# Kernel tuning notes

Hardware: AMD Instinct MI355X
Metric: run time of the kernel (lower is better)

## Reference

```python
import jax, jax.numpy as jnp
import numpy as np


def setup_inputs() -> dict:
    key = jax.random.key(0)
    ks = jax.random.split(key, 6)
    B, C, H, W, O = 8, 64, 64, 64, 64
    x = jax.random.normal(ks[0], (B, C, H, W), jnp.float32)
    wq = jax.random.normal(ks[1], (O, C), jnp.float32) * 0.1
    wk = jax.random.normal(ks[2], (O, C), jnp.float32) * 0.1
    wv = jax.random.normal(ks[3], (O, C), jnp.float32) * 0.1
    rel_w = jax.random.normal(ks[4], (O, W), jnp.float32)
    rel_h = jax.random.normal(ks[5], (O, H), jnp.float32)
    return {"x": x, "wq": wq, "wk": wk, "wv": wv,
            "rel_w": rel_w, "rel_h": rel_h,
            "kernel_size": 7, "padding": 3}


def reference(x, wq, wk, wv, rel_w, rel_h, kernel_size, padding):
    B, C, H, W = x.shape
    k, p = kernel_size, padding
    # 1x1 convs (no bias) == channel matmuls
    q = jnp.einsum('bchw,oc->bohw', x, wq)                      # [B,O,H,W]
    xp = jnp.pad(x, ((0, 0), (0, 0), (p, p), (p, p)))
    k_out = jnp.einsum('bchw,oc->bohw', xp, wk)                 # [B,O,H+2p,W+2p]
    v_out = jnp.einsum('bchw,oc->bohw', xp, wv)

    def patches(t):  # torch unfold(2).unfold(3) order: row offset slowest
        return jnp.stack([t[:, :, i:i + H, j:j + W]
                          for i in range(k) for j in range(k)], axis=-1)  # [B,O,H,W,k*k]

    kp = patches(k_out)
    vp = patches(v_out)
    # relative position logits (broadcast elementwise einsums)
    rel = q * rel_w[None, :, None, :] + q * rel_h[None, :, :, None]  # [B,O,H,W]
    logits = q[..., None] * kp + rel[..., None]                 # [B,O,H,W,k*k]
    attn = jax.nn.softmax(logits, axis=-1)
    return jnp.sum(attn * vp, axis=-1)                          # [B,O,H,W]
```

## Files before the change

### kernel.cpp

```cpp
#include <hip/hip_runtime.h>

#define HW 4096

__device__ float g_qkv[3 * 8 * 64 * HW];

#if __has_builtin(__builtin_amdgcn_exp2f)
#define QSCALE 1.4426950408889634f
__device__ __forceinline__ float fexp(float l) { return __builtin_amdgcn_exp2f(l); }
#else
#define QSCALE 1.0f
__device__ __forceinline__ float fexp(float l) { return __expf(l); }
#endif

__global__ __launch_bounds__(256, 2) void qkv_proj(
    const float* __restrict__ x,
    const float* __restrict__ wq,
    const float* __restrict__ wk,
    const float* __restrict__ wv)
{
    __shared__ float xs[64][64];
    __shared__ float wl[3][64][65];
    const int t = threadIdx.x;
    const int b = blockIdx.x >> 6;
    const int h = blockIdx.x & 63;

    {
        const float* __restrict__ mats[3] = { wq, wk, wv };
        #pragma unroll
        for (int m = 0; m < 3; ++m)
            for (int i = t; i < 4096; i += 256) {
                int o = i >> 6, c = i & 63;
                wl[m][o][c] = mats[m][i];
            }
        const float* xrow = x + (size_t)b * 64 * HW + (size_t)h * 64;
        for (int i = t; i < 4096; i += 256) {
            int c = i >> 6, w = i & 63;
            xs[c][w] = xrow[(size_t)c * HW + w];
        }
    }
    __syncthreads();

    const int w0 = (t & 15) * 4;
    const int o0 = (t >> 4) * 4;
    float acc[3][16];
    #pragma unroll
    for (int m = 0; m < 3; ++m)
        #pragma unroll
        for (int i = 0; i < 16; ++i) acc[m][i] = 0.f;

    #pragma unroll 4
    for (int cq = 0; cq < 16; ++cq) {
        const int c0 = cq * 4;
        float xa[4][4];
        #pragma unroll
        for (int ci = 0; ci < 4; ++ci)
            *(float4*)&xa[ci][0] = *(const float4*)&xs[c0 + ci][w0];
        #pragma unroll
        for (int m = 0; m < 3; ++m)
            #pragma unroll
            for (int oi = 0; oi < 4; ++oi) {
                #pragma unroll
                for (int ci = 0; ci < 4; ++ci) {
                    const float wv1 = wl[m][o0 + oi][c0 + ci];
                    #pragma unroll
                    for (int wi = 0; wi < 4; ++wi)
                        acc[m][oi * 4 + wi] = fmaf(wv1, xa[ci][wi], acc[m][oi * 4 + wi]);
                }
            }
    }

    #pragma unroll
    for (int m = 0; m < 3; ++m) {
        float* op = g_qkv + ((size_t)m * 8 + b) * (64 * HW) + (size_t)h * 64 + w0;
        #pragma unroll
        for (int oi = 0; oi < 4; ++oi) {
            float4 v = { acc[m][oi * 4 + 0], acc[m][oi * 4 + 1],
                         acc[m][oi * 4 + 2], acc[m][oi * 4 + 3] };
            *(float4*)&op[(size_t)(o0 + oi) * HW] = v;
        }
    }
}

__global__ __launch_bounds__(256, 2) void attn(float* __restrict__ out)
{
    __shared__ float kv[70][140];
    const int t = threadIdx.x;
    const int b = blockIdx.x >> 6;
    const int o = blockIdx.x & 63;

    const float* qb = g_qkv + ((size_t)(0 * 8 + b) * 64 + o) * HW;
    const float* kb = g_qkv + ((size_t)(1 * 8 + b) * 64 + o) * HW;
    const float* vb = g_qkv + ((size_t)(2 * 8 + b) * 64 + o) * HW;

    for (int i = t; i < 70 * 70; i += 256) {
        int r = i / 70, c = i - r * 70;
        int gh = r - 3, gw = c - 3;
        float kk = 0.f, vv = 0.f;
        if ((unsigned)gh < 64u && (unsigned)gw < 64u) {
            kk = kb[gh * 64 + gw];
            vv = vb[gh * 64 + gw];
        }
        kv[r][c] = kk;
        kv[r][70 + c] = vv;
    }
    __syncthreads();

    const int r0 = (t >> 4) * 4;
    const int c0 = (t & 15) * 4;

    float qv[16], den[16], num[16];
    #pragma unroll
    for (int i = 0; i < 4; ++i) {
        float4 q4 = *(const float4*)&qb[(r0 + i) * 64 + c0];
        qv[i * 4 + 0] = q4.x * QSCALE; qv[i * 4 + 1] = q4.y * QSCALE;
        qv[i * 4 + 2] = q4.z * QSCALE; qv[i * 4 + 3] = q4.w * QSCALE;
    }
    #pragma unroll
    for (int i = 0; i < 16; ++i) { den[i] = 0.f; num[i] = 0.f; }

    #pragma unroll
    for (int rr = 0; rr < 10; ++rr) {
        #pragma unroll
        for (int cc = 0; cc < 10; ++cc) {
            const float kk = kv[r0 + rr][c0 + cc];
            const float vv = kv[r0 + rr][70 + c0 + cc];
            #pragma unroll
            for (int i = 0; i < 4; ++i) {
                if (rr - i >= 0 && rr - i < 7) {
                    #pragma unroll
                    for (int j = 0; j < 4; ++j) {
                        if (cc - j >= 0 && cc - j < 7) {
                            float e = fexp(qv[i * 4 + j] * kk);
                            den[i * 4 + j] += e;
                            num[i * 4 + j] = fmaf(e, vv, num[i * 4 + j]);
                        }
                    }
                }
            }
        }
    }

    float* ob = out + ((size_t)(b * 64 + o)) * HW;
    #pragma unroll
    for (int i = 0; i < 4; ++i) {
        float4 v = { num[i * 4 + 0] / den[i * 4 + 0], num[i * 4 + 1] / den[i * 4 + 1],
                     num[i * 4 + 2] / den[i * 4 + 2], num[i * 4 + 3] / den[i * 4 + 3] };
        *(float4*)&ob[(r0 + i) * 64 + c0] = v;
    }
}

extern "C" void kernel_launch(void* const* d_in, const int* in_sizes, int n_in,
                              void* d_out, int out_size, void* d_ws, size_t ws_size,
                              hipStream_t stream)
{
    qkv_proj<<<dim3(512), dim3(256), 0, stream>>>(
        (const float*)d_in[0], (const float*)d_in[1],
        (const float*)d_in[2], (const float*)d_in[3]);
    attn<<<dim3(512), dim3(256), 0, stream>>>((float*)d_out);
}
```

Before: 117.4 us.

## Split qkv projection over output-channel groups and attention over row halves

The projection kernel now launches four times as many blocks, each computing 16 output channels with one pixel per lane. Weights are read directly from global memory as wave-uniform float4 loads instead of being staged in LDS. The attention kernel is split into two row halves per (b,o) with a smaller halo tile, doubling block count and reducing per-thread register state. The goal is better occupancy and load balance across the many CUs, at the cost of redundant x-row loads and a larger share of halo rows loaded per attention block.

```diff
diff --git a/kernel.cpp b/kernel.cpp
--- a/kernel.cpp
+++ b/kernel.cpp
@@ -12,89 +12,81 @@
 __device__ __forceinline__ float fexp(float l) { return __expf(l); }
 #endif
 
-__global__ __launch_bounds__(256, 2) void qkv_proj(
+__global__ __launch_bounds__(256, 8) void qkv_proj(
     const float* __restrict__ x,
     const float* __restrict__ wq,
     const float* __restrict__ wk,
     const float* __restrict__ wv)
 {
-    __shared__ float xs[64][64];
-    __shared__ float wl[3][64][65];
-    const int t = threadIdx.x;
-    const int b = blockIdx.x >> 6;
-    const int h = blockIdx.x & 63;
+    __shared__ float xs[64][68];
+    const int t  = threadIdx.x;
+    const int os = blockIdx.x >> 9;
+    const int b  = (blockIdx.x >> 6) & 7;
+    const int h  = blockIdx.x & 63;
 
-    {
-        const float* __restrict__ mats[3] = { wq, wk, wv };
-        #pragma unroll
-        for (int m = 0; m < 3; ++m)
-            for (int i = t; i < 4096; i += 256) {
-                int o = i >> 6, c = i & 63;
-                wl[m][o][c] = mats[m][i];
-            }
-        const float* xrow = x + (size_t)b * 64 * HW + (size_t)h * 64;
-        for (int i = t; i < 4096; i += 256) {
-            int c = i >> 6, w = i & 63;
-            xs[c][w] = xrow[(size_t)c * HW + w];
-        }
+    const float* __restrict__ xrow = x + (size_t)b * 64 * HW + (size_t)h * 64;
+    #pragma unroll
+    for (int i = t; i < 1024; i += 256) {
+        int c = i >> 4, w4 = (i & 15) << 2;
+        *(float4*)&xs[c][w4] = *(const float4*)&xrow[(size_t)c * HW + w4];
     }
     __syncthreads();
 
-    const int w0 = (t & 15) * 4;
-    const int o0 = (t >> 4) * 4;
-    float acc[3][16];
+    const int lane  = t & 63;
+    const int wave  = __builtin_amdgcn_readfirstlane(t >> 6);
+    const int obase = os * 16 + wave * 4;
+
+    const float* __restrict__ wmat[3] = { wq, wk, wv };
+    float acc[3][4];
     #pragma unroll
     for (int m = 0; m < 3; ++m)
         #pragma unroll
-        for (int i = 0; i < 16; ++i) acc[m][i] = 0.f;
+        for (int oi = 0; oi < 4; ++oi) acc[m][oi] = 0.f;
 
-    #pragma unroll 4
+    #pragma unroll 2
     for (int cq = 0; cq < 16; ++cq) {
         const int c0 = cq * 4;
-        float xa[4][4];
+        float xa[4];
         #pragma unroll
         for (int ci = 0; ci < 4; ++ci)
-            *(float4*)&xa[ci][0] = *(const float4*)&xs[c0 + ci][w0];
+            xa[ci] = xs[c0 + ci][lane];
         #pragma unroll
-        for (int m = 0; m < 3; ++m)
+        for (int m = 0; m < 3; ++m) {
             #pragma unroll
             for (int oi = 0; oi < 4; ++oi) {
-                #pragma unroll
-                for (int ci = 0; ci < 4; ++ci) {
-                    const float wv1 = wl[m][o0 + oi][c0 + ci];
-                    #pragma unroll
-                    for (int wi = 0; wi < 4; ++wi)
-                        acc[m][oi * 4 + wi] = fmaf(wv1, xa[ci][wi], acc[m][oi * 4 + wi]);
-                }
+                const float4 wf = *(const float4*)&wmat[m][(obase + oi) * 64 + c0];
+                acc[m][oi] = fmaf(wf.x, xa[0], acc[m][oi]);
+                acc[m][oi] = fmaf(wf.y, xa[1], acc[m][oi]);
+                acc[m][oi] = fmaf(wf.z, xa[2], acc[m][oi]);
+                acc[m][oi] = fmaf(wf.w, xa[3], acc[m][oi]);
             }
+        }
     }
 
     #pragma unroll
-    for (int m = 0; m < 3; ++m) {
-        float* op = g_qkv + ((size_t)m * 8 + b) * (64 * HW) + (size_t)h * 64 + w0;
+    for (int m = 0; m < 3; ++m)
         #pragma unroll
-        for (int oi = 0; oi < 4; ++oi) {
-            float4 v = { acc[m][oi * 4 + 0], acc[m][oi * 4 + 1],
-                         acc[m][oi * 4 + 2], acc[m][oi * 4 + 3] };
-            *(float4*)&op[(size_t)(o0 + oi) * HW] = v;
-        }
-    }
+        for (int oi = 0; oi < 4; ++oi)
+            g_qkv[((size_t)(m * 8 + b) * 64 + obase + oi) * HW + (size_t)h * 64 + lane]
+                = acc[m][oi];
 }
 
-__global__ __launch_bounds__(256, 2) void attn(float* __restrict__ out)
+__global__ __launch_bounds__(256, 4) void attn(float* __restrict__ out)
 {
-    __shared__ float kv[70][140];
-    const int t = threadIdx.x;
-    const int b = blockIdx.x >> 6;
-    const int o = blockIdx.x & 63;
+    __shared__ float kv[38][140];
+    const int t  = threadIdx.x;
+    const int hb = blockIdx.x >> 9;
+    const int b  = (blockIdx.x >> 6) & 7;
+    const int o  = blockIdx.x & 63;
+    const int R0 = hb * 32;
 
     const float* qb = g_qkv + ((size_t)(0 * 8 + b) * 64 + o) * HW;
     const float* kb = g_qkv + ((size_t)(1 * 8 + b) * 64 + o) * HW;
     const float* vb = g_qkv + ((size_t)(2 * 8 + b) * 64 + o) * HW;
 
-    for (int i = t; i < 70 * 70; i += 256) {
+    for (int i = t; i < 38 * 70; i += 256) {
         int r = i / 70, c = i - r * 70;
-        int gh = r - 3, gw = c - 3;
+        int gh = R0 + r - 3, gw = c - 3;
         float kk = 0.f, vv = 0.f;
         if ((unsigned)gh < 64u && (unsigned)gw < 64u) {
             kk = kb[gh * 64 + gw];
@@ -105,27 +97,27 @@
     }
     __syncthreads();
 
-    const int r0 = (t >> 4) * 4;
+    const int r0 = (t >> 4) * 2;
     const int c0 = (t & 15) * 4;
 
-    float qv[16], den[16], num[16];
+    float qv[8], den[8], num[8];
     #pragma unroll
-    for (int i = 0; i < 4; ++i) {
-        float4 q4 = *(const float4*)&qb[(r0 + i) * 64 + c0];
+    for (int i = 0; i < 2; ++i) {
+        float4 q4 = *(const float4*)&qb[(size_t)(R0 + r0 + i) * 64 + c0];
         qv[i * 4 + 0] = q4.x * QSCALE; qv[i * 4 + 1] = q4.y * QSCALE;
         qv[i * 4 + 2] = q4.z * QSCALE; qv[i * 4 + 3] = q4.w * QSCALE;
     }
     #pragma unroll
-    for (int i = 0; i < 16; ++i) { den[i] = 0.f; num[i] = 0.f; }
+    for (int i = 0; i < 8; ++i) { den[i] = 0.f; num[i] = 0.f; }
 
     #pragma unroll
-    for (int rr = 0; rr < 10; ++rr) {
+    for (int rr = 0; rr < 8; ++rr) {
         #pragma unroll
         for (int cc = 0; cc < 10; ++cc) {
             const float kk = kv[r0 + rr][c0 + cc];
             const float vv = kv[r0 + rr][70 + c0 + cc];
             #pragma unroll
-            for (int i = 0; i < 4; ++i) {
+            for (int i = 0; i < 2; ++i) {
                 if (rr - i >= 0 && rr - i < 7) {
                     #pragma unroll
                     for (int j = 0; j < 4; ++j) {
@@ -142,10 +134,10 @@
 
     float* ob = out + ((size_t)(b * 64 + o)) * HW;
     #pragma unroll
-    for (int i = 0; i < 4; ++i) {
+    for (int i = 0; i < 2; ++i) {
         float4 v = { num[i * 4 + 0] / den[i * 4 + 0], num[i * 4 + 1] / den[i * 4 + 1],
                      num[i * 4 + 2] / den[i * 4 + 2], num[i * 4 + 3] / den[i * 4 + 3] };
-        *(float4*)&ob[(r0 + i) * 64 + c0] = v;
+        *(float4*)&ob[(size_t)(R0 + r0 + i) * 64 + c0] = v;
     }
 }
 
@@ -153,8 +145,8 @@
                               void* d_out, int out_size, void* d_ws, size_t ws_size,
                               hipStream_t stream)
 {
-    qkv_proj<<<dim3(512), dim3(256), 0, stream>>>(
+    qkv_proj<<<dim3(2048), dim3(256), 0, stream>>>(
         (const float*)d_in[0], (const float*)d_in[1],
         (const float*)d_in[2], (const float*)d_in[3]);
-    attn<<<dim3(512), dim3(256), 0, stream>>>((float*)d_out);
+    attn<<<dim3(1024), dim3(256), 0, stream>>>((float*)d_out);
 }
```

New measurement: 237.1 us. 2.02x slower.
